# Kernel optimization log

Hardware: AMD Instinct MI355X
Metric: run time of the kernel (lower is better)

## Reference

```python
import jax, jax.numpy as jnp
import numpy as np

N, E = 50000, 800000
IN_CH, OUT_CH = 128, 16
H1, D1 = 2, 2 * OUT_CH           # conv1: heads=2, per-head dim 32, concat -> 64
MID = H1 * D1                    # 64
NEG_SLOPE = 0.2

def setup_inputs() -> dict:
    key = jax.random.key(0)
    ks = jax.random.split(key, 16)
    s = lambda k, shape: jax.random.normal(k, shape, dtype=jnp.float32) * 0.1
    return {
        "x": jax.random.normal(ks[0], (N, IN_CH), dtype=jnp.float32),
        "edge_index": jax.random.randint(ks[1], (2, E), 0, N, dtype=jnp.int64),
        "W1": s(ks[2], (IN_CH, H1 * D1)),
        "att_src1": s(ks[3], (H1, D1)),
        "att_dst1": s(ks[4], (H1, D1)),
        "b1": jnp.zeros((MID,), jnp.float32),
        "W_mu": s(ks[5], (MID, OUT_CH)),
        "att_src_mu": s(ks[6], (1, OUT_CH)),
        "att_dst_mu": s(ks[7], (1, OUT_CH)),
        "b_mu": jnp.zeros((OUT_CH,), jnp.float32),
        "W_ls": s(ks[8], (MID, OUT_CH)),
        "att_src_ls": s(ks[9], (1, OUT_CH)),
        "att_dst_ls": s(ks[10], (1, OUT_CH)),
        "b_ls": jnp.zeros((OUT_CH,), jnp.float32),
    }

def gat_conv(x, src, dst, W, att_src, att_dst, bias, heads, d):
    # x: [N, F]; src/dst: [E'] (self loops included); PyG GATConv, eval mode (dropout off)
    n = x.shape[0]
    h = (x @ W).reshape(n, heads, d)                     # [N, H, D]
    a_src = jnp.sum(h * att_src, axis=-1)                # [N, H]
    a_dst = jnp.sum(h * att_dst, axis=-1)                # [N, H]
    e = jax.nn.leaky_relu(a_src[src] + a_dst[dst], NEG_SLOPE)   # [E', H]
    # segment softmax over incoming edges of each destination node
    m = jax.ops.segment_max(e, dst, num_segments=n)
    ex = jnp.exp(e - m[dst])
    denom = jax.ops.segment_sum(ex, dst, num_segments=n)
    alpha = ex / (denom[dst] + 1e-16)                    # [E', H]
    msg = h[src] * alpha[:, :, None]                     # [E', H, D]
    out = jax.ops.segment_sum(msg, dst, num_segments=n)  # [N, H, D]
    return out, bias

def reference(x, edge_index, W1, att_src1, att_dst1, b1,
              W_mu, att_src_mu, att_dst_mu, b_mu,
              W_ls, att_src_ls, att_dst_ls, b_ls):
    n = x.shape[0]
    loops = jnp.arange(n, dtype=edge_index.dtype)
    src = jnp.concatenate([edge_index[0], loops])        # add_self_loops=True (inputs have none)
    dst = jnp.concatenate([edge_index[1], loops])
    h, b = gat_conv(x, src, dst, W1, att_src1, att_dst1, b1, H1, D1)
    h = jax.nn.relu(h.reshape(n, H1 * D1) + b)           # concat=True -> [N, 64]
    mu, bm = gat_conv(h, src, dst, W_mu, att_src_mu, att_dst_mu, b_mu, 1, OUT_CH)
    ls, bl = gat_conv(h, src, dst, W_ls, att_src_ls, att_dst_ls, b_ls, 1, OUT_CH)
    mu = mu.mean(axis=1) + bm                            # concat=False, heads=1 -> mean == squeeze
    ls = ls.mean(axis=1) + bl
    return (mu, ls)
```

## Files before the change

### kernel.cpp

```cpp
#include <hip/hip_runtime.h>

#define NEG 0.2f

__device__ __forceinline__ float lrelu(float v) { return v > 0.f ? v : NEG * v; }

__device__ __forceinline__ unsigned short f2bf(float f) {
    unsigned u = __float_as_uint(f);
    unsigned r = (u + 0x7FFF + ((u >> 16) & 1)) >> 16;
    return (unsigned short)r;
}
__device__ __forceinline__ float bf_lo(unsigned v) { return __uint_as_float(v << 16); }
__device__ __forceinline__ float bf_hi(unsigned v) { return __uint_as_float(v & 0xffff0000u); }

__global__ void build_w1ext(const float* __restrict__ W1, const float* __restrict__ asrc,
                            const float* __restrict__ adst, float* __restrict__ Wext) {
    int i = blockIdx.x * blockDim.x + threadIdx.x;
    if (i >= 128 * 80) return;
    int k = i / 80, c = i % 80;
    if (c < 64) { Wext[i] = W1[k * 64 + c]; return; }
    if (c >= 68) { Wext[i] = 0.f; return; }
    int j = c - 64;
    int hh = j & 1;
    const float* att = (j >= 2) ? adst : asrc;
    float s = 0.f;
    for (int d = 0; d < 32; ++d) s += W1[k * 64 + hh * 32 + d] * att[hh * 32 + d];
    Wext[i] = s;
}

__global__ void build_w2ext(const float* __restrict__ Wmu, const float* __restrict__ Wls,
                            const float* __restrict__ asmu, const float* __restrict__ admu,
                            const float* __restrict__ asls, const float* __restrict__ adls,
                            float* __restrict__ Wext) {
    int i = blockIdx.x * blockDim.x + threadIdx.x;
    if (i >= 64 * 36) return;
    int k = i / 36, c = i % 36;
    if (c < 16) { Wext[i] = Wmu[k * 16 + c]; return; }
    if (c < 32) { Wext[i] = Wls[k * 16 + (c - 16)]; return; }
    int j = c - 32;
    const float* W = (j < 2) ? Wmu : Wls;
    const float* att = (j == 0) ? asmu : (j == 1) ? admu : (j == 2) ? asls : adls;
    float s = 0.f;
    for (int c2 = 0; c2 < 16; ++c2) s += W[k * 16 + c2] * att[c2];
    Wext[i] = s;
}

__global__ __launch_bounds__(320) void gemm1(const float* __restrict__ x,
                                             const float* __restrict__ Wext,
                                             unsigned* __restrict__ h32, float* __restrict__ a1, int n) {
    __shared__ float xs[64][132];
    __shared__ float Ws[128][80];
    int t = threadIdx.x;
    int row0 = blockIdx.x * 64;
    for (int i = t; i < 128 * 20; i += 320) {
        int r = i / 20, cq = i % 20;
        *(float4*)&Ws[r][cq * 4] = *(const float4*)&Wext[r * 80 + cq * 4];
    }
    for (int i = t; i < 64 * 32; i += 320) {
        int r = i >> 5, kq = i & 31;
        int gr = row0 + r;
        float4 v = (gr < n) ? *(const float4*)&x[gr * 128 + kq * 4] : make_float4(0, 0, 0, 0);
        *(float4*)&xs[r][kq * 4] = v;
    }
    __syncthreads();
    int rg = t / 20, cg = t % 20;
    int r0 = rg * 4, c0 = cg * 4;
    float4 acc0 = make_float4(0, 0, 0, 0), acc1 = acc0, acc2 = acc0, acc3 = acc0;
    for (int k = 0; k < 128; k += 4) {
        float4 w0 = *(float4*)&Ws[k + 0][c0];
        float4 w1 = *(float4*)&Ws[k + 1][c0];
        float4 w2 = *(float4*)&Ws[k + 2][c0];
        float4 w3 = *(float4*)&Ws[k + 3][c0];
#pragma unroll
        for (int j = 0; j < 4; ++j) {
            float4 xv = *(float4*)&xs[r0 + j][k];
            float4& a = j == 0 ? acc0 : j == 1 ? acc1 : j == 2 ? acc2 : acc3;
            a.x += xv.x * w0.x + xv.y * w1.x + xv.z * w2.x + xv.w * w3.x;
            a.y += xv.x * w0.y + xv.y * w1.y + xv.z * w2.y + xv.w * w3.y;
            a.z += xv.x * w0.z + xv.y * w1.z + xv.z * w2.z + xv.w * w3.z;
            a.w += xv.x * w0.w + xv.y * w1.w + xv.z * w2.w + xv.w * w3.w;
        }
    }
#pragma unroll
    for (int j = 0; j < 4; ++j) {
        int gr = row0 + r0 + j;
        if (gr >= n) break;
        float4 a = j == 0 ? acc0 : j == 1 ? acc1 : j == 2 ? acc2 : acc3;
        if (cg < 16) {
            unsigned p0 = ((unsigned)f2bf(a.y) << 16) | f2bf(a.x);
            unsigned p1 = ((unsigned)f2bf(a.w) << 16) | f2bf(a.z);
            *(uint2*)&h32[gr * 32 + (c0 >> 1)] = make_uint2(p0, p1);
        } else if (cg == 16) {
            *(float4*)&a1[gr * 4] = a;
        }
    }
}

__global__ __launch_bounds__(256) void count_deg_part(const int* __restrict__ dstv, int E, int np,
                                                      int* __restrict__ deg) {
    int p = blockIdx.x & 7;
    int bslot = blockIdx.x >> 3;
    int nblk = gridDim.x >> 3;
    int lo = p * np, hi = lo + np;
    for (int i = bslot * 256 + threadIdx.x; i < E; i += nblk * 256) {
        int d = dstv[i];
        if (d >= lo && d < hi) atomicAdd(&deg[d], 1);
    }
}

__global__ __launch_bounds__(256) void scatter_part(const int* __restrict__ srcv,
                                                    const int* __restrict__ dstv, int E, int np,
                                                    int* __restrict__ cursor, int* __restrict__ srcs) {
    int p = blockIdx.x & 7;
    int bslot = blockIdx.x >> 3;
    int nblk = gridDim.x >> 3;
    int lo = p * np, hi = lo + np;
    for (int i = bslot * 256 + threadIdx.x; i < E; i += nblk * 256) {
        int d = dstv[i];
        if (d >= lo && d < hi) {
            int slot = atomicAdd(&cursor[d], 1);
            srcs[slot] = srcv[i];
        }
    }
}

__global__ __launch_bounds__(256) void block_sums(const int* __restrict__ deg, int n,
                                                  int* __restrict__ bsums) {
    int i = blockIdx.x * 256 + threadIdx.x;
    int v = (i < n) ? deg[i] : 0;
    for (int o = 32; o > 0; o >>= 1) v += __shfl_down(v, o, 64);
    __shared__ int ws[4];
    if ((threadIdx.x & 63) == 0) ws[threadIdx.x >> 6] = v;
    __syncthreads();
    if (threadIdx.x == 0) bsums[blockIdx.x] = ws[0] + ws[1] + ws[2] + ws[3];
}

__global__ __launch_bounds__(256) void scan_bsums(int* __restrict__ bsums, int nb) {
    __shared__ int s[256];
    int t = threadIdx.x;
    int v = (t < nb) ? bsums[t] : 0;
    s[t] = v;
    __syncthreads();
    for (int o = 1; o < 256; o <<= 1) {
        int u = (t >= o) ? s[t - o] : 0;
        __syncthreads();
        s[t] += u;
        __syncthreads();
    }
    if (t < nb) bsums[t] = s[t] - v;
}

__global__ __launch_bounds__(256) void write_offs(const int* __restrict__ deg,
                                                  const int* __restrict__ bsums, int n,
                                                  int* __restrict__ offs, int* __restrict__ cursor) {
    int t = threadIdx.x;
    int i = blockIdx.x * 256 + t;
    int v = (i < n) ? deg[i] : 0;
    __shared__ int s[256];
    s[t] = v;
    __syncthreads();
    for (int o = 1; o < 256; o <<= 1) {
        int u = (t >= o) ? s[t - o] : 0;
        __syncthreads();
        s[t] += u;
        __syncthreads();
    }
    int excl = s[t] - v + bsums[blockIdx.x];
    if (i < n) { offs[i] = excl; cursor[i] = excl; }
    if (i == n - 1) offs[n] = excl + v;
}

__global__ __launch_bounds__(256) void agg1(const unsigned* __restrict__ h32, const float* __restrict__ a1,
                                            const int* __restrict__ offs, const int* __restrict__ srcs,
                                            const float* __restrict__ b1, float* __restrict__ h1, int n) {
    int wid = threadIdx.x >> 6, lane = threadIdx.x & 63;
    int node = blockIdx.x * 4 + wid;
    if (node >= n) return;
    int q = lane >> 4;
    int l = lane & 15;
    int head = l >> 3;
    float adst = a1[node * 4 + 2 + head];
    float ax = 0.f, ay = 0.f, az = 0.f, aw = 0.f, denom = 0.f;
    if (q == 0) {
        float w = __expf(lrelu(a1[node * 4 + head] + adst));
        uint2 hv = *(const uint2*)&h32[node * 32 + 2 * l];
        ax = w * bf_lo(hv.x); ay = w * bf_hi(hv.x);
        az = w * bf_lo(hv.y); aw = w * bf_hi(hv.y);
        denom = w;
    }
    int kb = offs[node], ke = offs[node + 1];
    for (int k = kb + q; k < ke; k += 4) {
        int s = srcs[k];
        float wv = __expf(lrelu(a1[s * 4 + head] + adst));
        uint2 hv = *(const uint2*)&h32[s * 32 + 2 * l];
        denom += wv;
        ax += wv * bf_lo(hv.x); ay += wv * bf_hi(hv.x);
        az += wv * bf_lo(hv.y); aw += wv * bf_hi(hv.y);
    }
    ax += __shfl_xor(ax, 16, 64); ax += __shfl_xor(ax, 32, 64);
    ay += __shfl_xor(ay, 16, 64); ay += __shfl_xor(ay, 32, 64);
    az += __shfl_xor(az, 16, 64); az += __shfl_xor(az, 32, 64);
    aw += __shfl_xor(aw, 16, 64); aw += __shfl_xor(aw, 32, 64);
    denom += __shfl_xor(denom, 16, 64); denom += __shfl_xor(denom, 32, 64);
    if (q == 0) {
        float4 bv = *(const float4*)&b1[4 * l];
        float4 o;
        o.x = fmaxf(ax / denom + bv.x, 0.f);
        o.y = fmaxf(ay / denom + bv.y, 0.f);
        o.z = fmaxf(az / denom + bv.z, 0.f);
        o.w = fmaxf(aw / denom + bv.w, 0.f);
        *(float4*)&h1[node * 64 + 4 * l] = o;
    }
}

__global__ __launch_bounds__(256) void gemm2(const float* __restrict__ h1,
                                             const float* __restrict__ Wext,
                                             unsigned* __restrict__ hml, float* __restrict__ a2, int n) {
    __shared__ float hs[16][65];
    __shared__ float Ws[64][36];
    int t = threadIdx.x;
    int row0 = blockIdx.x * 16;
    for (int i = t; i < 64 * 36; i += 256) Ws[i / 36][i % 36] = Wext[i];
    for (int i = t; i < 16 * 64; i += 256) {
        int r = i >> 6, k = i & 63;
        int gr = row0 + r;
        hs[r][k] = (gr < n) ? h1[gr * 64 + k] : 0.f;
    }
    __syncthreads();
    int r = t >> 4, c = t & 15;
    float am = 0, al = 0;
    for (int k = 0; k < 64; ++k) {
        float hv = hs[r][k];
        am += hv * Ws[k][c];
        al += hv * Ws[k][16 + c];
    }
    int gr = row0 + r;
    if (gr < n) hml[gr * 16 + c] = ((unsigned)f2bf(al) << 16) | f2bf(am);
    if (t < 64) {
        int r2 = t >> 2, j = t & 3;
        float a = 0.f;
        for (int k = 0; k < 64; ++k) a += hs[r2][k] * Ws[k][32 + j];
        if (row0 + r2 < n) a2[(row0 + r2) * 4 + j] = a;
    }
}

__global__ __launch_bounds__(256) void agg2(const unsigned* __restrict__ hml,
                                            const float* __restrict__ a2, const int* __restrict__ offs,
                                            const int* __restrict__ srcs,
                                            const float* __restrict__ bmu, const float* __restrict__ bls,
                                            float* __restrict__ out, int n) {
    int wid = threadIdx.x >> 6, lane = threadIdx.x & 63;
    int node = blockIdx.x * 4 + wid;
    if (node >= n) return;
    int q = lane >> 4, c = lane & 15;
    float admu = a2[node * 4 + 1], adls = a2[node * 4 + 3];
    float amu = 0.f, als = 0.f, dmu = 0.f, dls = 0.f;
    if (q == 0) {
        float wmu = __expf(lrelu(a2[node * 4 + 0] + admu));
        float wls = __expf(lrelu(a2[node * 4 + 2] + adls));
        unsigned hv = hml[node * 16 + c];
        amu = wmu * bf_lo(hv); als = wls * bf_hi(hv);
        dmu = wmu; dls = wls;
    }
    int kb = offs[node], ke = offs[node + 1];
    for (int k = kb + q; k < ke; k += 4) {
        int s = srcs[k];
        float4 av = *(const float4*)&a2[s * 4];
        float w1v = __expf(lrelu(av.x + admu));
        float w2v = __expf(lrelu(av.z + adls));
        unsigned hv = hml[s * 16 + c];
        dmu += w1v; dls += w2v;
        amu += w1v * bf_lo(hv);
        als += w2v * bf_hi(hv);
    }
    amu += __shfl_xor(amu, 16, 64); amu += __shfl_xor(amu, 32, 64);
    als += __shfl_xor(als, 16, 64); als += __shfl_xor(als, 32, 64);
    dmu += __shfl_xor(dmu, 16, 64); dmu += __shfl_xor(dmu, 32, 64);
    dls += __shfl_xor(dls, 16, 64); dls += __shfl_xor(dls, 32, 64);
    if (q == 0) {
        out[node * 16 + c] = amu / dmu + bmu[c];
        out[(size_t)n * 16 + node * 16 + c] = als / dls + bls[c];
    }
}

extern "C" void kernel_launch(void* const* d_in, const int* in_sizes, int n_in,
                              void* d_out, int out_size, void* d_ws, size_t ws_size,
                              hipStream_t stream) {
    const float* x    = (const float*)d_in[0];
    const int*   ei   = (const int*)d_in[1];
    const float* W1   = (const float*)d_in[2];
    const float* as1  = (const float*)d_in[3];
    const float* ad1  = (const float*)d_in[4];
    const float* b1   = (const float*)d_in[5];
    const float* Wmu  = (const float*)d_in[6];
    const float* asmu = (const float*)d_in[7];
    const float* admu = (const float*)d_in[8];
    const float* bmu  = (const float*)d_in[9];
    const float* Wls  = (const float*)d_in[10];
    const float* asls = (const float*)d_in[11];
    const float* adls = (const float*)d_in[12];
    const float* bls  = (const float*)d_in[13];
    float* out = (float*)d_out;

    int n = in_sizes[0] / 128;
    int E = in_sizes[1] / 2;
    int np = (n + 7) / 8;

    char* ws = (char*)d_ws;
    size_t off = 0;
    auto alloc = [&](size_t b) { size_t p = off; off = (off + b + 255) & ~(size_t)255; return p; };

    unsigned* h32 = (unsigned*)(ws + alloc((size_t)n * 32 * 4));
    float*    h1  = (float*)(ws + alloc((size_t)n * 64 * 4));
    float*    a1  = (float*)(ws + alloc((size_t)n * 4 * 4));
    unsigned* hml = (unsigned*)(ws + alloc((size_t)n * 16 * 4));
    float*    a2  = (float*)(ws + alloc((size_t)n * 4 * 4));
    float*    w1e = (float*)(ws + alloc(128 * 80 * 4));
    float*    w2e = (float*)(ws + alloc(64 * 36 * 4));
    int*   deg    = (int*)(ws + alloc((size_t)n * 4));
    int*   offs   = (int*)(ws + alloc((size_t)(n + 1) * 4));
    int*   cursor = (int*)(ws + alloc((size_t)n * 4));
    int*   srcs   = (int*)(ws + alloc((size_t)E * 4));
    int*   bsums  = (int*)(ws + alloc(1024 * 4));

    int nb = (n + 255) / 256;

    hipMemsetAsync(deg, 0, (size_t)n * 4, stream);
    build_w1ext<<<(128 * 80 + 255) / 256, 256, 0, stream>>>(W1, as1, ad1, w1e);
    build_w2ext<<<(64 * 36 + 255) / 256, 256, 0, stream>>>(Wmu, Wls, asmu, admu, asls, adls, w2e);
    gemm1<<<(n + 63) / 64, 320, 0, stream>>>(x, w1e, h32, a1, n);
    count_deg_part<<<2048, 256, 0, stream>>>(ei + E, E, np, deg);
    block_sums<<<nb, 256, 0, stream>>>(deg, n, bsums);
    scan_bsums<<<1, 256, 0, stream>>>(bsums, nb);
    write_offs<<<nb, 256, 0, stream>>>(deg, bsums, n, offs, cursor);
    scatter_part<<<2048, 256, 0, stream>>>(ei, ei + E, E, np, cursor, srcs);
    agg1<<<(n + 3) / 4, 256, 0, stream>>>(h32, a1, offs, srcs, b1, h1, n);
    gemm2<<<(n + 15) / 16, 256, 0, stream>>>(h1, w2e, hml, a2, n);
    agg2<<<(n + 3) / 4, 256, 0, stream>>>(hml, a2, offs, srcs, bmu, bls, out, n);
}
```

Before: 304.2 us.

## Move both dense GEMMs onto bf16 MFMA with split-precision weights

Replaces the shared-memory FP32 SIMT GEMMs for layer 1 and layer 2 with MFMA 16x16x32 bf16 instructions. Precision is kept close to FP32 by splitting activations and weights into hi/lo bf16 parts and summing the cross terms. Weights are pre-transposed to column-major bf16. agg1 now writes its output as bf16, which halves the bytes gemm2 reads. The intent is to cut ALU and LDS cost in the GEMM stages. The costs are extra MFMA passes, lost precision in h1 (gemm2 uses only the hi part of the activations), and uncoalesced 2-byte stores.

```diff
diff --git a/kernel.cpp b/kernel.cpp
--- a/kernel.cpp
+++ b/kernel.cpp
@@ -1,6 +1,9 @@
 #include <hip/hip_runtime.h>
 
 #define NEG 0.2f
+
+typedef __attribute__((ext_vector_type(8))) short short8;
+typedef __attribute__((ext_vector_type(4))) float f32x4;
 
 __device__ __forceinline__ float lrelu(float v) { return v > 0.f ? v : NEG * v; }
 
@@ -9,89 +12,142 @@
     unsigned r = (u + 0x7FFF + ((u >> 16) & 1)) >> 16;
     return (unsigned short)r;
 }
+__device__ __forceinline__ float bf2f(unsigned short h) { return __uint_as_float((unsigned)h << 16); }
 __device__ __forceinline__ float bf_lo(unsigned v) { return __uint_as_float(v << 16); }
 __device__ __forceinline__ float bf_hi(unsigned v) { return __uint_as_float(v & 0xffff0000u); }
 
 __global__ void build_w1ext(const float* __restrict__ W1, const float* __restrict__ asrc,
-                            const float* __restrict__ adst, float* __restrict__ Wext) {
+                            const float* __restrict__ adst,
+                            unsigned short* __restrict__ Wt_hi, unsigned short* __restrict__ Wt_lo) {
     int i = blockIdx.x * blockDim.x + threadIdx.x;
     if (i >= 128 * 80) return;
     int k = i / 80, c = i % 80;
-    if (c < 64) { Wext[i] = W1[k * 64 + c]; return; }
-    if (c >= 68) { Wext[i] = 0.f; return; }
-    int j = c - 64;
-    int hh = j & 1;
-    const float* att = (j >= 2) ? adst : asrc;
-    float s = 0.f;
-    for (int d = 0; d < 32; ++d) s += W1[k * 64 + hh * 32 + d] * att[hh * 32 + d];
-    Wext[i] = s;
+    float val;
+    if (c < 64) val = W1[k * 64 + c];
+    else if (c < 68) {
+        int j = c - 64;
+        int hh = j & 1;
+        const float* att = (j >= 2) ? adst : asrc;
+        float s = 0.f;
+        for (int d = 0; d < 32; ++d) s += W1[k * 64 + hh * 32 + d] * att[hh * 32 + d];
+        val = s;
+    } else val = 0.f;
+    unsigned short h = f2bf(val);
+    Wt_hi[c * 128 + k] = h;
+    Wt_lo[c * 128 + k] = f2bf(val - bf2f(h));
 }
 
 __global__ void build_w2ext(const float* __restrict__ Wmu, const float* __restrict__ Wls,
                             const float* __restrict__ asmu, const float* __restrict__ admu,
                             const float* __restrict__ asls, const float* __restrict__ adls,
-                            float* __restrict__ Wext) {
+                            unsigned short* __restrict__ Wt_hi, unsigned short* __restrict__ Wt_lo) {
     int i = blockIdx.x * blockDim.x + threadIdx.x;
-    if (i >= 64 * 36) return;
-    int k = i / 36, c = i % 36;
-    if (c < 16) { Wext[i] = Wmu[k * 16 + c]; return; }
-    if (c < 32) { Wext[i] = Wls[k * 16 + (c - 16)]; return; }
-    int j = c - 32;
-    const float* W = (j < 2) ? Wmu : Wls;
-    const float* att = (j == 0) ? asmu : (j == 1) ? admu : (j == 2) ? asls : adls;
-    float s = 0.f;
-    for (int c2 = 0; c2 < 16; ++c2) s += W[k * 16 + c2] * att[c2];
-    Wext[i] = s;
-}
-
-__global__ __launch_bounds__(320) void gemm1(const float* __restrict__ x,
-                                             const float* __restrict__ Wext,
-                                             unsigned* __restrict__ h32, float* __restrict__ a1, int n) {
-    __shared__ float xs[64][132];
-    __shared__ float Ws[128][80];
-    int t = threadIdx.x;
-    int row0 = blockIdx.x * 64;
-    for (int i = t; i < 128 * 20; i += 320) {
-        int r = i / 20, cq = i % 20;
-        *(float4*)&Ws[r][cq * 4] = *(const float4*)&Wext[r * 80 + cq * 4];
-    }
-    for (int i = t; i < 64 * 32; i += 320) {
-        int r = i >> 5, kq = i & 31;
-        int gr = row0 + r;
-        float4 v = (gr < n) ? *(const float4*)&x[gr * 128 + kq * 4] : make_float4(0, 0, 0, 0);
-        *(float4*)&xs[r][kq * 4] = v;
-    }
-    __syncthreads();
-    int rg = t / 20, cg = t % 20;
-    int r0 = rg * 4, c0 = cg * 4;
-    float4 acc0 = make_float4(0, 0, 0, 0), acc1 = acc0, acc2 = acc0, acc3 = acc0;
-    for (int k = 0; k < 128; k += 4) {
-        float4 w0 = *(float4*)&Ws[k + 0][c0];
-        float4 w1 = *(float4*)&Ws[k + 1][c0];
-        float4 w2 = *(float4*)&Ws[k + 2][c0];
-        float4 w3 = *(float4*)&Ws[k + 3][c0];
-#pragma unroll
-        for (int j = 0; j < 4; ++j) {
-            float4 xv = *(float4*)&xs[r0 + j][k];
-            float4& a = j == 0 ? acc0 : j == 1 ? acc1 : j == 2 ? acc2 : acc3;
-            a.x += xv.x * w0.x + xv.y * w1.x + xv.z * w2.x + xv.w * w3.x;
-            a.y += xv.x * w0.y + xv.y * w1.y + xv.z * w2.y + xv.w * w3.y;
-            a.z += xv.x * w0.z + xv.y * w1.z + xv.z * w2.z + xv.w * w3.z;
-            a.w += xv.x * w0.w + xv.y * w1.w + xv.z * w2.w + xv.w * w3.w;
+    if (i >= 64 * 48) return;
+    int k = i / 48, c = i % 48;
+    float val;
+    if (c < 16) val = Wmu[k * 16 + c];
+    else if (c < 32) val = Wls[k * 16 + (c - 16)];
+    else if (c < 36) {
+        int j = c - 32;
+        const float* W = (j < 2) ? Wmu : Wls;
+        const float* att = (j == 0) ? asmu : (j == 1) ? admu : (j == 2) ? asls : adls;
+        float s = 0.f;
+        for (int c2 = 0; c2 < 16; ++c2) s += W[k * 16 + c2] * att[c2];
+        val = s;
+    } else val = 0.f;
+    unsigned short h = f2bf(val);
+    Wt_hi[c * 64 + k] = h;
+    Wt_lo[c * 64 + k] = f2bf(val - bf2f(h));
+}
+
+__global__ __launch_bounds__(256) void gemm1(const float* __restrict__ x,
+                                             const unsigned short* __restrict__ Wt_hi,
+                                             const unsigned short* __restrict__ Wt_lo,
+                                             unsigned short* __restrict__ hbf,
+                                             float* __restrict__ a1, int n) {
+    int wid = threadIdx.x >> 6, lane = threadIdx.x & 63;
+    int m = lane & 15, b = lane >> 4;
+    int row = blockIdx.x * 64 + wid * 16 + m;
+    int rowc = min(row, n - 1);
+    short8 ah[4], al[4];
+    const float* xp = x + (size_t)rowc * 128 + b * 8;
+#pragma unroll
+    for (int kc = 0; kc < 4; ++kc) {
+        float4 v0 = *(const float4*)(xp + kc * 32);
+        float4 v1 = *(const float4*)(xp + kc * 32 + 4);
+        float vv[8] = {v0.x, v0.y, v0.z, v0.w, v1.x, v1.y, v1.z, v1.w};
+#pragma unroll
+        for (int j = 0; j < 8; ++j) {
+            unsigned short h = f2bf(vv[j]);
+            ah[kc][j] = (short)h;
+            al[kc][j] = (short)f2bf(vv[j] - bf2f(h));
         }
     }
+    int orow0 = blockIdx.x * 64 + wid * 16 + b * 4;
+#pragma unroll
+    for (int ct = 0; ct < 5; ++ct) {
+        f32x4 acc = {0.f, 0.f, 0.f, 0.f};
+        int col = ct * 16 + m;
+        const unsigned short* wh = Wt_hi + col * 128 + b * 8;
+        const unsigned short* wl = Wt_lo + col * 128 + b * 8;
+#pragma unroll
+        for (int kc = 0; kc < 4; ++kc) {
+            short8 bh = *(const short8*)(wh + kc * 32);
+            short8 bl = *(const short8*)(wl + kc * 32);
+            acc = __builtin_amdgcn_mfma_f32_16x16x32_bf16(ah[kc], bh, acc, 0, 0, 0);
+            acc = __builtin_amdgcn_mfma_f32_16x16x32_bf16(al[kc], bh, acc, 0, 0, 0);
+            acc = __builtin_amdgcn_mfma_f32_16x16x32_bf16(ah[kc], bl, acc, 0, 0, 0);
+        }
+        if (ct < 4) {
+#pragma unroll
+            for (int j = 0; j < 4; ++j) {
+                int orow = orow0 + j;
+                if (orow < n) hbf[(size_t)orow * 64 + ct * 16 + m] = f2bf(acc[j]);
+            }
+        } else if (m < 4) {
+#pragma unroll
+            for (int j = 0; j < 4; ++j) {
+                int orow = orow0 + j;
+                if (orow < n) a1[(size_t)orow * 4 + m] = acc[j];
+            }
+        }
+    }
+}
+
+__global__ __launch_bounds__(256) void gemm2(const unsigned short* __restrict__ h1bf,
+                                             const unsigned short* __restrict__ Wt_hi,
+                                             const unsigned short* __restrict__ Wt_lo,
+                                             unsigned* __restrict__ hml, float* __restrict__ a2, int n) {
+    int wid = threadIdx.x >> 6, lane = threadIdx.x & 63;
+    int m = lane & 15, b = lane >> 4;
+    int row = blockIdx.x * 64 + wid * 16 + m;
+    int rowc = min(row, n - 1);
+    short8 a0 = *(const short8*)(h1bf + (size_t)rowc * 64 + b * 8);
+    short8 a1f = *(const short8*)(h1bf + (size_t)rowc * 64 + 32 + b * 8);
+    int orow0 = blockIdx.x * 64 + wid * 16 + b * 4;
+    f32x4 accs[3];
+#pragma unroll
+    for (int ct = 0; ct < 3; ++ct) {
+        f32x4 acc = {0.f, 0.f, 0.f, 0.f};
+        int col = ct * 16 + m;
+        const unsigned short* wh = Wt_hi + col * 64 + b * 8;
+        const unsigned short* wl = Wt_lo + col * 64 + b * 8;
+        short8 bh0 = *(const short8*)(wh);
+        short8 bl0 = *(const short8*)(wl);
+        short8 bh1 = *(const short8*)(wh + 32);
+        short8 bl1 = *(const short8*)(wl + 32);
+        acc = __builtin_amdgcn_mfma_f32_16x16x32_bf16(a0, bh0, acc, 0, 0, 0);
+        acc = __builtin_amdgcn_mfma_f32_16x16x32_bf16(a0, bl0, acc, 0, 0, 0);
+        acc = __builtin_amdgcn_mfma_f32_16x16x32_bf16(a1f, bh1, acc, 0, 0, 0);
+        acc = __builtin_amdgcn_mfma_f32_16x16x32_bf16(a1f, bl1, acc, 0, 0, 0);
+        accs[ct] = acc;
+    }
 #pragma unroll
     for (int j = 0; j < 4; ++j) {
-        int gr = row0 + r0 + j;
-        if (gr >= n) break;
-        float4 a = j == 0 ? acc0 : j == 1 ? acc1 : j == 2 ? acc2 : acc3;
-        if (cg < 16) {
-            unsigned p0 = ((unsigned)f2bf(a.y) << 16) | f2bf(a.x);
-            unsigned p1 = ((unsigned)f2bf(a.w) << 16) | f2bf(a.z);
-            *(uint2*)&h32[gr * 32 + (c0 >> 1)] = make_uint2(p0, p1);
-        } else if (cg == 16) {
-            *(float4*)&a1[gr * 4] = a;
-        }
+        int orow = orow0 + j;
+        if (orow >= n) break;
+        hml[(size_t)orow * 16 + m] = ((unsigned)f2bf(accs[1][j]) << 16) | f2bf(accs[0][j]);
+        if (m < 4) a2[(size_t)orow * 4 + m] = accs[2][j];
     }
 }
 
@@ -171,7 +227,7 @@
 
 __global__ __launch_bounds__(256) void agg1(const unsigned* __restrict__ h32, const float* __restrict__ a1,
                                             const int* __restrict__ offs, const int* __restrict__ srcs,
-                                            const float* __restrict__ b1, float* __restrict__ h1, int n) {
+                                            const float* __restrict__ b1, unsigned* __restrict__ h1u, int n) {
     int wid = threadIdx.x >> 6, lane = threadIdx.x & 63;
     int node = blockIdx.x * 4 + wid;
     if (node >= n) return;
@@ -203,43 +259,14 @@
     denom += __shfl_xor(denom, 16, 64); denom += __shfl_xor(denom, 32, 64);
     if (q == 0) {
         float4 bv = *(const float4*)&b1[4 * l];
-        float4 o;
-        o.x = fmaxf(ax / denom + bv.x, 0.f);
-        o.y = fmaxf(ay / denom + bv.y, 0.f);
-        o.z = fmaxf(az / denom + bv.z, 0.f);
-        o.w = fmaxf(aw / denom + bv.w, 0.f);
-        *(float4*)&h1[node * 64 + 4 * l] = o;
-    }
-}
-
-__global__ __launch_bounds__(256) void gemm2(const float* __restrict__ h1,
-                                             const float* __restrict__ Wext,
-                                             unsigned* __restrict__ hml, float* __restrict__ a2, int n) {
-    __shared__ float hs[16][65];
-    __shared__ float Ws[64][36];
-    int t = threadIdx.x;
-    int row0 = blockIdx.x * 16;
-    for (int i = t; i < 64 * 36; i += 256) Ws[i / 36][i % 36] = Wext[i];
-    for (int i = t; i < 16 * 64; i += 256) {
-        int r = i >> 6, k = i & 63;
-        int gr = row0 + r;
-        hs[r][k] = (gr < n) ? h1[gr * 64 + k] : 0.f;
-    }
-    __syncthreads();
-    int r = t >> 4, c = t & 15;
-    float am = 0, al = 0;
-    for (int k = 0; k < 64; ++k) {
-        float hv = hs[r][k];
-        am += hv * Ws[k][c];
-        al += hv * Ws[k][16 + c];
-    }
-    int gr = row0 + r;
-    if (gr < n) hml[gr * 16 + c] = ((unsigned)f2bf(al) << 16) | f2bf(am);
-    if (t < 64) {
-        int r2 = t >> 2, j = t & 3;
-        float a = 0.f;
-        for (int k = 0; k < 64; ++k) a += hs[r2][k] * Ws[k][32 + j];
-        if (row0 + r2 < n) a2[(row0 + r2) * 4 + j] = a;
+        float o0 = fmaxf(ax / denom + bv.x, 0.f);
+        float o1 = fmaxf(ay / denom + bv.y, 0.f);
+        float o2 = fmaxf(az / denom + bv.z, 0.f);
+        float o3 = fmaxf(aw / denom + bv.w, 0.f);
+        uint2 o;
+        o.x = ((unsigned)f2bf(o1) << 16) | f2bf(o0);
+        o.y = ((unsigned)f2bf(o3) << 16) | f2bf(o2);
+        *(uint2*)&h1u[node * 32 + 2 * l] = o;
     }
 }
 
@@ -309,13 +336,15 @@
     size_t off = 0;
     auto alloc = [&](size_t b) { size_t p = off; off = (off + b + 255) & ~(size_t)255; return p; };
 
-    unsigned* h32 = (unsigned*)(ws + alloc((size_t)n * 32 * 4));
-    float*    h1  = (float*)(ws + alloc((size_t)n * 64 * 4));
-    float*    a1  = (float*)(ws + alloc((size_t)n * 4 * 4));
-    unsigned* hml = (unsigned*)(ws + alloc((size_t)n * 16 * 4));
-    float*    a2  = (float*)(ws + alloc((size_t)n * 4 * 4));
-    float*    w1e = (float*)(ws + alloc(128 * 80 * 4));
-    float*    w2e = (float*)(ws + alloc(64 * 36 * 4));
+    unsigned short* hbf  = (unsigned short*)(ws + alloc((size_t)n * 64 * 2));
+    unsigned*       h1u  = (unsigned*)(ws + alloc((size_t)n * 32 * 4));
+    float*          a1   = (float*)(ws + alloc((size_t)n * 4 * 4));
+    unsigned*       hml  = (unsigned*)(ws + alloc((size_t)n * 16 * 4));
+    float*          a2   = (float*)(ws + alloc((size_t)n * 4 * 4));
+    unsigned short* w1h  = (unsigned short*)(ws + alloc(80 * 128 * 2));
+    unsigned short* w1l  = (unsigned short*)(ws + alloc(80 * 128 * 2));
+    unsigned short* w2h  = (unsigned short*)(ws + alloc(48 * 64 * 2));
+    unsigned short* w2l  = (unsigned short*)(ws + alloc(48 * 64 * 2));
     int*   deg    = (int*)(ws + alloc((size_t)n * 4));
     int*   offs   = (int*)(ws + alloc((size_t)(n + 1) * 4));
     int*   cursor = (int*)(ws + alloc((size_t)n * 4));
@@ -325,15 +354,15 @@
     int nb = (n + 255) / 256;
 
     hipMemsetAsync(deg, 0, (size_t)n * 4, stream);
-    build_w1ext<<<(128 * 80 + 255) / 256, 256, 0, stream>>>(W1, as1, ad1, w1e);
-    build_w2ext<<<(64 * 36 + 255) / 256, 256, 0, stream>>>(Wmu, Wls, asmu, admu, asls, adls, w2e);
-    gemm1<<<(n + 63) / 64, 320, 0, stream>>>(x, w1e, h32, a1, n);
+    build_w1ext<<<(128 * 80 + 255) / 256, 256, 0, stream>>>(W1, as1, ad1, w1h, w1l);
+    build_w2ext<<<(64 * 48 + 255) / 256, 256, 0, stream>>>(Wmu, Wls, asmu, admu, asls, adls, w2h, w2l);
+    gemm1<<<(n + 63) / 64, 256, 0, stream>>>(x, w1h, w1l, hbf, a1, n);
     count_deg_part<<<2048, 256, 0, stream>>>(ei + E, E, np, deg);
     block_sums<<<nb, 256, 0, stream>>>(deg, n, bsums);
     scan_bsums<<<1, 256, 0, stream>>>(bsums, nb);
     write_offs<<<nb, 256, 0, stream>>>(deg, bsums, n, offs, cursor);
     scatter_part<<<2048, 256, 0, stream>>>(ei, ei + E, E, np, cursor, srcs);
-    agg1<<<(n + 3) / 4, 256, 0, stream>>>(h32, a1, offs, srcs, b1, h1, n);
-    gemm2<<<(n + 15) / 16, 256, 0, stream>>>(h1, w2e, hml, a2, n);
+    agg1<<<(n + 3) / 4, 256, 0, stream>>>((const unsigned*)hbf, a1, offs, srcs, b1, h1u, n);
+    gemm2<<<(n + 63) / 64, 256, 0, stream>>>((const unsigned short*)h1u, w2h, w2l, hml, a2, n);
     agg2<<<(n + 3) / 4, 256, 0, stream>>>(hml, a2, offs, srcs, bmu, bls, out, n);
 }
```

Result: faster. 277.1 us (-8.9%).
